# Optimization experiments

Hardware: AMD Instinct MI355X
Metric: run time of the kernel (lower is better)

The kernel has to match this reference:

```python
import jax, jax.numpy as jnp
import numpy as np

N = 2048      # num graph nodes (activities + places)
D = 256       # embedding_size
C = 3 * D     # cat_embedding_size
V = 2         # num variants
L = 16        # activities per variant
E = 16 * N    # edges for the encoder GNN
DEG_P = 0.0156  # adjacency density (~32 out-degree)


def setup_inputs() -> dict:
    key = jax.random.key(0)
    ks = jax.random.split(key, 6)
    embeddings = jax.random.normal(ks[0], (N, D), dtype=jnp.float32)
    W_self = jax.random.normal(ks[1], (D, D), dtype=jnp.float32) * 0.05
    W_nbr = jax.random.normal(ks[2], (D, D), dtype=jnp.float32) * 0.05
    b = jnp.zeros((D,), dtype=jnp.float32)
    variants = jax.random.randint(ks[3], (V, L), 0, N, dtype=jnp.int32)
    original = (jax.random.uniform(ks[4], (N, N)) < DEG_P).astype(jnp.int32)
    edge_index = jax.random.randint(ks[5], (2, E), 0, N, dtype=jnp.int32)
    return {"embeddings": embeddings, "W_self": W_self, "W_nbr": W_nbr, "b": b,
            "variants": variants, "original": original, "edge_index": edge_index}


def _forward(embeddings, W_self, W_nbr, b, variants, original, edge_index):
    n, d = embeddings.shape
    c = 3 * d
    dt = embeddings.dtype
    adj = original.astype(dt)              # [N,N]; adj[i,j]=1 iff edge i->j (forward star = row)
    src_e, dst_e = edge_index[0], edge_index[1]

    def encoder(x):
        # SecondEncoder approximated as one GCN-style message-passing layer
        msg = jax.ops.segment_sum(x[src_e], dst_e, num_segments=n)
        return jax.nn.relu(x @ W_self + msg @ W_nbr + b)

    def run_variant(acts):  # acts: [L] int32
        onehot = jax.nn.one_hot(acts, n, dtype=dt)                # [L,N]
        incl = jnp.flip(jnp.cumsum(jnp.flip(onehot, 0), 0), 0)    # sum_{j>=i} onehot[j]
        present_later = ((incl - onehot) > 0).astype(dt)          # set of nodes in acts[i+1:]

        def step(carry, inp):
            emb, pi, summary = carry
            a, plater = inp
            followers = adj[a]                                    # forward star of activity a
            has = jnp.any(followers > 0)
            adj_m = adj * plater[None, :]                         # edges into later-in-variant activities
            dest_cnt = adj_m.sum(axis=1)                          # |destination set| per candidate place
            dst_all = adj_m @ emb                                 # summed destination embeddings, [N,D]
            mask = jnp.where(has, ((followers > 0) & (dest_cnt > 0)).astype(dt), 0.0)
            # cat = (place_f, src_f, dst_f) per considered place
            cat = jnp.concatenate(
                [emb, jnp.broadcast_to(emb[a][None, :], emb.shape), dst_all], axis=1) * mask[:, None]
            pi = pi + cat                                         # places_info[place] += cat
            # prev_embedding_summary += places_info[place] for each considered place
            summary = summary + (mask[:, None] * pi).sum(axis=0)
            # places_info[considered] += prev_embedding_summary
            pi = pi + mask[:, None] * summary[None, :]
            emb = jnp.where(has, encoder(emb), emb)               # encoder skipped when no followers
            return (emb, pi, summary), None

        init = (embeddings, jnp.zeros((n, c), dt), jnp.zeros((c,), dt))
        (_, pi, _), _ = jax.lax.scan(step, init, (acts, present_later))
        return pi

    # variant shuffle in the original is irrelevant: embeddings reset each variant
    # and final_places_info is a sum over variants.
    return jax.vmap(run_variant)(variants).sum(axis=0)


def reference(embeddings, W_self, W_nbr, b, variants, original, edge_index):
    return _forward(embeddings, W_self, W_nbr, b, variants, original, edge_index)
```

## Files before the change

kernel.cpp:

```cpp
#include <hip/hip_runtime.h>

#define N 2048
#define D 256
#define C 768
#define V 2
#define L 16
#define NSTATE 15
#define NAPP 14
#define TCAP 256
#define FCAP 64

typedef __attribute__((ext_vector_type(8))) short bf16x8;
typedef __attribute__((ext_vector_type(4))) float f32x4;

__device__ __forceinline__ ushort bf16_rn(float x) {
  unsigned u = __float_as_uint(x);
  u += 0x7FFFu + ((u >> 16) & 1u);
  return (ushort)(u >> 16);
}
__device__ __forceinline__ float bf16_f(ushort h) {
  return __uint_as_float(((unsigned)h) << 16);
}

__device__ __forceinline__ size_t a_addr(int row, int k) {
  return ((size_t)(row >> 5) * 4 + (k >> 6)) * 2048 + (row & 31) * 64 + (k & 63);
}
__device__ __forceinline__ size_t wt_addr(int n, int k) {
  return ((size_t)(n >> 5) * 4 + (k >> 6)) * 2048 + (n & 31) * 64 + (k & 63);
}

__global__ __launch_bounds__(256) void k_init(
    const float* __restrict__ emb, const float* __restrict__ Ws,
    const float* __restrict__ Wn, float* __restrict__ states0,
    ushort* __restrict__ WtHi, ushort* __restrict__ WtLo,
    ushort* __restrict__ A0hi, ushort* __restrict__ A0lo,
    float* __restrict__ out, int* __restrict__ fillpos) {
  size_t i = (size_t)blockIdx.x * 256 + threadIdx.x;
  size_t stride = (size_t)gridDim.x * 256;
  for (size_t x = i; x < (size_t)N * D; x += stride) {
    float v = emb[x];
    states0[x] = v;
    ushort h = bf16_rn(v);
    ushort l = bf16_rn(v - bf16_f(h));
    size_t a = a_addr((int)(x >> 8), (int)(x & 255));
    A0hi[a] = h;
    A0lo[a] = l;
  }
  for (size_t x = i; x < (size_t)512 * 256; x += stride) {
    int n = (int)(x >> 8), k = (int)(x & 255);
    float v = (n < 256) ? Ws[(size_t)k * 256 + n] : Wn[(size_t)k * 256 + (n - 256)];
    ushort h = bf16_rn(v);
    size_t a = wt_addr(n, k);
    WtHi[a] = h;
    WtLo[a] = bf16_rn(v - bf16_f(h));
  }
  for (size_t x = i; x < (size_t)N * C; x += stride) out[x] = 0.f;
  for (size_t x = i; x < N; x += stride) fillpos[x] = 0;
}

__global__ void k_deg(const int* __restrict__ ei, int* __restrict__ fillpos, int E) {
  int e = blockIdx.x * 256 + threadIdx.x;
  if (e < E) atomicAdd(&fillpos[ei[E + e]], 1);
}

__global__ __launch_bounds__(256) void k_scan(int* __restrict__ fillpos,
                                              int* __restrict__ row_ptr) {
  __shared__ int part[256];
  __shared__ int base[257];
  int t = threadIdx.x;
  int v[8];
  int s = 0;
  for (int j = 0; j < 8; j++) { v[j] = fillpos[t * 8 + j]; s += v[j]; }
  part[t] = s;
  __syncthreads();
  if (t == 0) {
    int acc = 0;
    for (int q = 0; q < 256; q++) { base[q] = acc; acc += part[q]; }
    base[256] = acc;
  }
  __syncthreads();
  int acc = base[t];
  for (int j = 0; j < 8; j++) {
    row_ptr[t * 8 + j] = acc;
    fillpos[t * 8 + j] = acc;
    acc += v[j];
  }
  if (t == 255) row_ptr[N] = base[256];
}

__global__ void k_fill(const int* __restrict__ ei, int* __restrict__ fillpos,
                       int* __restrict__ csr_src, int E) {
  int e = blockIdx.x * 256 + threadIdx.x;
  if (e < E) {
    int dst = ei[E + e];
    int pos = atomicAdd(&fillpos[dst], 1);
    csr_src[pos] = ei[e];
  }
}

__global__ __launch_bounds__(256) void k_metaA(
    const int* __restrict__ adj, const int* __restrict__ variants,
    int* __restrict__ stepP, int* __restrict__ stepDm,
    int* __restrict__ stepCnt, int* __restrict__ hasG, int* __restrict__ tlG) {
  __shared__ int tl_sh[16];
  __shared__ int foll[FCAP], fbits[FCAP];
  __shared__ int sh_tc, sh_fcnt, sh_ecnt;
  int vi = blockIdx.x;
  int v = vi / L, i = vi % L;
  int t = threadIdx.x;
  int a = variants[vi];
  if (t == 0) {
    int cnt = 0;
    for (int j = i + 1; j < L; j++) {
      int x = variants[v * L + j];
      bool dup = false;
      for (int q = 0; q < cnt; q++) if (tl_sh[q] == x) dup = true;
      if (!dup) tl_sh[cnt++] = x;
    }
    sh_tc = cnt;
    sh_fcnt = 0;
    sh_ecnt = 0;
    for (int q = 0; q < cnt; q++) tlG[vi * 16 + q] = tl_sh[q];
  }
  __syncthreads();
  for (int p = t; p < N; p += 256) {
    if (adj[(size_t)a * N + p] != 0) {
      int f = atomicAdd(&sh_fcnt, 1);
      if (f < FCAP) foll[f] = p;
    }
  }
  __syncthreads();
  int fc = sh_fcnt < FCAP ? sh_fcnt : FCAP;
  int tc = sh_tc;
  for (int x = t; x < fc; x += 256) fbits[x] = 0;
  __syncthreads();
  for (int x = t; x < fc * tc; x += 256) {
    int fi = x / tc, q = x - fi * tc;
    if (adj[(size_t)foll[fi] * N + tl_sh[q]] != 0) atomicOr(&fbits[fi], 1 << q);
  }
  __syncthreads();
  for (int fi = t; fi < fc; fi += 256) {
    int bits = fbits[fi];
    if (bits) {
      int e = atomicAdd(&sh_ecnt, 1);
      stepP[vi * FCAP + e] = foll[fi];
      stepDm[vi * FCAP + e] = bits;
    }
  }
  __syncthreads();
  if (t == 0) {
    stepCnt[vi] = sh_ecnt;
    hasG[vi] = (sh_fcnt > 0);
  }
}

__global__ __launch_bounds__(256) void k_metaB(
    const int* __restrict__ stepP, const int* __restrict__ stepDm,
    const int* __restrict__ stepCnt, const int* __restrict__ hasG,
    int* __restrict__ entP, int* __restrict__ entPrev, int* __restrict__ entDm,
    int* __restrict__ offsG, int* __restrict__ kidxG, int* __restrict__ cmatG,
    int* __restrict__ lastPG, int* __restrict__ lastIG, int* __restrict__ lastMG,
    int* __restrict__ cntG) {
  __shared__ int pmask[N];
  __shared__ int sP[16][FCAP];
  __shared__ int sDm[16][FCAP];
  __shared__ int cnt[16], offs[17];
  __shared__ int cmat_sh[256];
  __shared__ int sh_u;
  int v = blockIdx.x, t = threadIdx.x;
  for (int p = t; p < N; p += 256) pmask[p] = 0;
  for (int x = t; x < 256; x += 256) cmat_sh[x] = 0;
  if (t < 16) cnt[t] = stepCnt[v * L + t];
  if (t == 0) sh_u = 0;
  __syncthreads();
  if (t == 0) {
    int acc = 0;
    for (int i = 0; i < 16; i++) {
      offs[i] = acc < TCAP ? acc : TCAP;
      acc += cnt[i];
    }
    offs[16] = acc < TCAP ? acc : TCAP;
    cntG[v * 2 + 0] = offs[16];
    int k = 0;
    for (int i = 0; i < L; i++) {
      kidxG[v * 16 + i] = k;
      if (hasG[v * L + i]) k++;
    }
  }
  for (int x = t; x < 16 * FCAP; x += 256) {
    int i = x >> 6, f = x & 63;
    if (f < stepCnt[v * L + i]) {
      int p = stepP[(v * L + i) * FCAP + f];
      sP[i][f] = p;
      sDm[i][f] = stepDm[(v * L + i) * FCAP + f];
      atomicOr(&pmask[p], 1 << i);
    }
  }
  __syncthreads();
  for (int x = t; x < 16 * FCAP; x += 256) {
    int i = x >> 6, f = x & 63;
    if (f < cnt[i]) {
      int e = offs[i] + f;
      if (e < TCAP) {
        int p = sP[i][f];
        entP[v * TCAP + e] = p;
        entDm[v * TCAP + e] = sDm[i][f];
        int m = pmask[p] & ((1 << i) - 1);
        int prev = -1;
        if (m) {
          int j = 31 - __clz(m);
          int cj = cnt[j];
          for (int f2 = 0; f2 < cj; f2++)
            if (sP[j][f2] == p) { prev = offs[j] + f2; break; }
        }
        entPrev[v * TCAP + e] = prev;
      }
    }
  }
  __syncthreads();
  for (int p = t; p < N; p += 256) {
    int m = pmask[p];
    if (m) {
      int u = atomicAdd(&sh_u, 1);
      int j = 31 - __clz(m);
      int li = -1;
      int cj = cnt[j];
      for (int f2 = 0; f2 < cj; f2++)
        if (sP[j][f2] == p) { li = offs[j] + f2; break; }
      lastPG[v * TCAP + u] = p;
      lastIG[v * TCAP + u] = li;
      lastMG[v * TCAP + u] = m;
      int mm = m;
      while (mm) {
        int bi = __ffs(mm) - 1; mm &= mm - 1;
        int m2 = m & ((1 << bi) - 1);
        while (m2) {
          int bj = __ffs(m2) - 1; m2 &= m2 - 1;
          atomicAdd(&cmat_sh[bi * 16 + bj], 1);
        }
      }
    }
  }
  __syncthreads();
  if (t == 0) cntG[v * 2 + 1] = sh_u;
  for (int x = t; x < 256; x += 256) cmatG[v * 256 + x] = cmat_sh[x];
  for (int x = t; x < 17; x += 256) offsG[v * 17 + x] = offs[x];
}

__global__ __launch_bounds__(256) void k_gemm(
    const ushort* __restrict__ Ah, const ushort* __restrict__ Al,
    const ushort* __restrict__ Wh_g, const ushort* __restrict__ Wl_g,
    float* __restrict__ Z) {
  __shared__ __align__(16) ushort Ash[32][72], Asl[32][72];
  __shared__ __align__(16) ushort Wsh[32][72], Wsl[32][72];
  const int tid = threadIdx.x, wave = tid >> 6, lane = tid & 63;
  const int quad = lane >> 4, l16 = lane & 15;
  const int wr = wave >> 1, wc = wave & 1;
  const int mb = blockIdx.x, nb = blockIdx.y;
  const int sr = tid >> 3, sc = (tid & 7) * 8;

  f32x4 acc = {0.f, 0.f, 0.f, 0.f};
  size_t abase = (size_t)mb * 4 * 2048 + (size_t)tid * 8;
  size_t wbase = (size_t)nb * 4 * 2048 + (size_t)tid * 8;
  uint4 ra  = *(const uint4*)&Ah[abase];
  uint4 rl  = *(const uint4*)&Al[abase];
  uint4 rwh = *(const uint4*)&Wh_g[wbase];
  uint4 rwl = *(const uint4*)&Wl_g[wbase];
#pragma unroll
  for (int c = 0; c < 4; c++) {
    *(uint4*)&Ash[sr][sc] = ra;
    *(uint4*)&Asl[sr][sc] = rl;
    *(uint4*)&Wsh[sr][sc] = rwh;
    *(uint4*)&Wsl[sr][sc] = rwl;
    __syncthreads();
    if (c < 3) {
      size_t o = (size_t)(c + 1) * 2048;
      ra  = *(const uint4*)&Ah[abase + o];
      rl  = *(const uint4*)&Al[abase + o];
      rwh = *(const uint4*)&Wh_g[wbase + o];
      rwl = *(const uint4*)&Wl_g[wbase + o];
    }
#pragma unroll
    for (int kf = 0; kf < 2; kf++) {
      int ko = kf * 32 + quad * 8;
      bf16x8 a_h = *(const bf16x8*)&Ash[wr * 16 + l16][ko];
      bf16x8 a_l = *(const bf16x8*)&Asl[wr * 16 + l16][ko];
      bf16x8 w_h = *(const bf16x8*)&Wsh[wc * 16 + l16][ko];
      bf16x8 w_l = *(const bf16x8*)&Wsl[wc * 16 + l16][ko];
      acc = __builtin_amdgcn_mfma_f32_16x16x32_bf16(a_h, w_h, acc, 0, 0, 0);
      acc = __builtin_amdgcn_mfma_f32_16x16x32_bf16(a_h, w_l, acc, 0, 0, 0);
      acc = __builtin_amdgcn_mfma_f32_16x16x32_bf16(a_l, w_h, acc, 0, 0, 0);
    }
    __syncthreads();
  }
  int col = nb * 32 + wc * 16 + l16;
  int row0 = mb * 32 + wr * 16 + quad * 4;
#pragma unroll
  for (int r = 0; r < 4; r++)
    Z[(size_t)(row0 + r) * 512 + col] = acc[r];
}

__global__ __launch_bounds__(256) void k_comb(
    const float* __restrict__ Z, const float* __restrict__ bias,
    const int* __restrict__ row_ptr, const int* __restrict__ csr_src,
    float* __restrict__ stnext, ushort* __restrict__ NAh,
    ushort* __restrict__ NAl) {
  __shared__ float4 part[2][64];
  int wid = threadIdx.x >> 6, lane = threadIdx.x & 63;
  int rp = wid >> 1, half = wid & 1;
  int row = blockIdx.x * 2 + rp;
  int e0 = row_ptr[row], e1 = row_ptr[row + 1];
  int mid = (e0 + e1 + 1) >> 1;
  int lo = half ? mid : e0, hi = half ? e1 : mid;
  float4 acc = {0.f, 0.f, 0.f, 0.f};
  for (int e = lo; e < hi; e++) {
    const float4* z2 = (const float4*)(Z + (size_t)csr_src[e] * 512 + 256);
    float4 x = z2[lane];
    acc.x += x.x; acc.y += x.y; acc.z += x.z; acc.w += x.w;
  }
  if (half) part[rp][lane] = acc;
  __syncthreads();
  if (!half) {
    float4 o = part[rp][lane];
    float4 zs = ((const float4*)(Z + (size_t)row * 512))[lane];
    float4 bv = ((const float4*)bias)[lane];
    float v0 = fmaxf(acc.x + o.x + zs.x + bv.x, 0.f);
    float v1 = fmaxf(acc.y + o.y + zs.y + bv.y, 0.f);
    float v2 = fmaxf(acc.z + o.z + zs.z + bv.z, 0.f);
    float v3 = fmaxf(acc.w + o.w + zs.w + bv.w, 0.f);
    *(float4*)(stnext + (size_t)row * D + lane * 4) = make_float4(v0, v1, v2, v3);
    ushort h0 = bf16_rn(v0), h1 = bf16_rn(v1), h2 = bf16_rn(v2), h3 = bf16_rn(v3);
    size_t ca = a_addr(row, lane * 4);
    *(ushort4*)&NAh[ca] = make_ushort4(h0, h1, h2, h3);
    *(ushort4*)&NAl[ca] = make_ushort4(
        bf16_rn(v0 - bf16_f(h0)), bf16_rn(v1 - bf16_f(h1)),
        bf16_rn(v2 - bf16_f(h2)), bf16_rn(v3 - bf16_f(h3)));
  }
}

#define PI_LDS_BYTES (TCAP * 64 * 4 + 16 * 64 * 4 + 3 * TCAP * 4 + 17 * 4 + 16 * 4 + 256 * 4)
__global__ __launch_bounds__(64) void k_pi(
    const float* __restrict__ states, float* __restrict__ out,
    const int* __restrict__ variants,
    const int* __restrict__ entP, const int* __restrict__ entPrev,
    const int* __restrict__ entDm, const int* __restrict__ offsG,
    const int* __restrict__ kidxG, const int* __restrict__ tlG,
    const int* __restrict__ cmatG, const int* __restrict__ lastPG,
    const int* __restrict__ lastIG, const int* __restrict__ lastMG,
    const int* __restrict__ cntG) {
  extern __shared__ __align__(16) float smf[];
  float* catb = smf;
  float* S_lds = catb + TCAP * 64;
  int* eP  = (int*)(S_lds + 16 * 64);
  int* ePr = eP + TCAP;
  int* eDm = ePr + TCAP;
  int* offs = eDm + TCAP;
  int* kidx = offs + 17;
  int* tl = kidx + 16;
  int v = blockIdx.x / 12, cgi = blockIdx.x % 12;
  int grp = cgi >> 2;
  int lane = threadIdx.x;
  int cl = (cgi & 3) * 64 + lane;
  int col = cgi * 64 + lane;

  int T = cntG[v * 2 + 0], U = cntG[v * 2 + 1];
  for (int x = lane; x < T; x += 64) {
    eP[x] = entP[v * TCAP + x];
    ePr[x] = entPrev[v * TCAP + x];
    eDm[x] = entDm[v * TCAP + x];
  }
  for (int x = lane; x < 17; x += 64) offs[x] = offsG[v * 17 + x];
  if (lane < 16) kidx[lane] = kidxG[v * 16 + lane];
  for (int x = lane; x < 256; x += 64) tl[x] = tlG[v * 256 + x];
  __syncthreads();

  for (int i = 0; i < L; i++) {
    int kk = kidx[i]; if (kk > NSTATE - 1) kk = NSTATE - 1;
    const float* embS = states + (size_t)kk * N * D;
    int o0 = offs[i], o1 = offs[i + 1];
    if (grp == 0) {
      for (int e = o0; e < o1; e++)
        catb[e * 64 + lane] = embS[(size_t)eP[e] * D + cl];
    } else if (grp == 1) {
      float embA = embS[(size_t)variants[v * L + i] * D + cl];
      for (int e = o0; e < o1; e++) catb[e * 64 + lane] = embA;
    } else {
      for (int e = o0; e < o1; e++) {
        float s = 0.f;
        int b = eDm[e];
        while (b) {
          int q = __ffs(b) - 1; b &= b - 1;
          s += embS[(size_t)tl[i * 16 + q] * D + cl];
        }
        catb[e * 64 + lane] = s;
      }
    }
  }
  for (int e = 0; e < T; e++) {
    int pr = ePr[e];
    if (pr >= 0) catb[e * 64 + lane] += catb[pr * 64 + lane];
  }
  float S[16];
  float Sp = 0.f;
#pragma unroll
  for (int i = 0; i < 16; i++) {
    float a = 0.f;
    for (int e = offs[i]; e < offs[i + 1]; e++) a += catb[e * 64 + lane];
    float s = Sp + a;
#pragma unroll
    for (int j = 0; j < 16; j++)
      if (j < i) s += (float)cmatG[v * 256 + i * 16 + j] * S[j];
    S[i] = s;
    S_lds[i * 64 + lane] = s;
    Sp = s;
  }
  for (int u = 0; u < U; u++) {
    int p = lastPG[v * TCAP + u];
    int li = lastIG[v * TCAP + u];
    int m = lastMG[v * TCAP + u];
    float acc = catb[li * 64 + lane];
    while (m) {
      int q = __ffs(m) - 1; m &= m - 1;
      acc += S_lds[q * 64 + lane];
    }
    atomicAdd(&out[(size_t)p * C + col], acc);
  }
}

extern "C" void kernel_launch(void* const* d_in, const int* in_sizes, int n_in,
                              void* d_out, int out_size, void* d_ws, size_t ws_size,
                              hipStream_t stream) {
  const float* emb      = (const float*)d_in[0];
  const float* Ws       = (const float*)d_in[1];
  const float* Wn       = (const float*)d_in[2];
  const float* bias     = (const float*)d_in[3];
  const int*   variants = (const int*)d_in[4];
  const int*   adj      = (const int*)d_in[5];
  const int*   ei       = (const int*)d_in[6];
  const int    E        = in_sizes[6] / 2;
  float* out            = (float*)d_out;

  char* base = (char*)d_ws;
  float* states = (float*)base;            base += (size_t)NSTATE * N * D * 4;
  float* Z      = (float*)base;            base += (size_t)N * 512 * 4;
  ushort* WtHi  = (ushort*)base;           base += (size_t)512 * 256 * 2;
  ushort* WtLo  = (ushort*)base;           base += (size_t)512 * 256 * 2;
  ushort* A0h   = (ushort*)base;           base += (size_t)N * D * 2;
  ushort* A0l   = (ushort*)base;           base += (size_t)N * D * 2;
  ushort* A1h   = (ushort*)base;           base += (size_t)N * D * 2;
  ushort* A1l   = (ushort*)base;           base += (size_t)N * D * 2;
  int* row_ptr  = (int*)base;              base += (N + 1) * 4;
  int* fillpos  = (int*)base;              base += N * 4;
  int* csr_src  = (int*)base;              base += (size_t)E * 4;
  int* stepP    = (int*)base;              base += V * L * FCAP * 4;
  int* stepDm   = (int*)base;              base += V * L * FCAP * 4;
  int* stepCnt  = (int*)base;              base += V * L * 4;
  int* hasG     = (int*)base;              base += V * L * 4;
  int* entP     = (int*)base;              base += V * TCAP * 4;
  int* entPrev  = (int*)base;              base += V * TCAP * 4;
  int* entDm    = (int*)base;              base += V * TCAP * 4;
  int* offsG    = (int*)base;              base += V * 17 * 4;
  int* kidxG    = (int*)base;              base += V * 16 * 4;
  int* tlG      = (int*)base;              base += V * 256 * 4;
  int* cmatG    = (int*)base;              base += V * 256 * 4;
  int* lastPG   = (int*)base;              base += V * TCAP * 4;
  int* lastIG   = (int*)base;              base += V * TCAP * 4;
  int* lastMG   = (int*)base;              base += V * TCAP * 4;
  int* cntG     = (int*)base;              base += V * 2 * 4;

  hipFuncSetAttribute((const void*)k_pi,
                      hipFuncAttributeMaxDynamicSharedMemorySize, PI_LDS_BYTES);

  k_init<<<512, 256, 0, stream>>>(emb, Ws, Wn, states, WtHi, WtLo, A0h, A0l,
                                  out, fillpos);
  k_deg<<<(E + 255) / 256, 256, 0, stream>>>(ei, fillpos, E);
  k_scan<<<1, 256, 0, stream>>>(fillpos, row_ptr);
  k_fill<<<(E + 255) / 256, 256, 0, stream>>>(ei, fillpos, csr_src, E);
  k_metaA<<<V * L, 256, 0, stream>>>(adj, variants, stepP, stepDm, stepCnt,
                                     hasG, tlG);
  k_metaB<<<V, 256, 0, stream>>>(stepP, stepDm, stepCnt, hasG, entP, entPrev,
                                 entDm, offsG, kidxG, cmatG, lastPG, lastIG,
                                 lastMG, cntG);

  ushort* AH[2] = {A0h, A1h};
  ushort* AL[2] = {A0l, A1l};
  for (int s = 0; s < NAPP; s++) {
    int cur = s & 1, nxt = cur ^ 1;
    k_gemm<<<dim3(64, 16), 256, 0, stream>>>(AH[cur], AL[cur], WtHi, WtLo, Z);
    k_comb<<<N / 2, 256, 0, stream>>>(Z, bias, row_ptr, csr_src,
                                      states + (size_t)(s + 1) * N * D,
                                      AH[nxt], AL[nxt]);
  }
  k_pi<<<V * 12, 64, PI_LDS_BYTES, stream>>>(states, out, variants, entP,
                                             entPrev, entDm, offsG, kidxG, tlG,
                                             cmatG, lastPG, lastIG, lastMG, cntG);
}
```

Measured before the change: 386.9 us.

## Merge setup kernels, double-buffer GEMM LDS, simplify per-row gather combine

Merges the degree-count kernel with the per-step metadata kernel, and the CSR fill kernel with the per-variant metadata kernel, by splitting blocks by index. This cuts the number of launches. The GEMM now double-buffers its LDS tiles, so each k-chunk needs one barrier instead of two. The combine kernel now runs one wave per row with two independent accumulators instead of splitting each row across two waves with an LDS reduction. The extra LDS in the GEMM and the loss of intra-row parallelism on high-degree rows may offset part of the benefit.

```diff
diff --git a/kernel.cpp b/kernel.cpp
--- a/kernel.cpp
+++ b/kernel.cpp
@@ -58,9 +58,66 @@
   for (size_t x = i; x < N; x += stride) fillpos[x] = 0;
 }
 
-__global__ void k_deg(const int* __restrict__ ei, int* __restrict__ fillpos, int E) {
-  int e = blockIdx.x * 256 + threadIdx.x;
-  if (e < E) atomicAdd(&fillpos[ei[E + e]], 1);
+__global__ __launch_bounds__(256) void k_degA(
+    const int* __restrict__ ei, int E, int* __restrict__ fillpos,
+    const int* __restrict__ adj, const int* __restrict__ variants,
+    int* __restrict__ stepP, int* __restrict__ stepDm,
+    int* __restrict__ stepCnt, int* __restrict__ hasG, int* __restrict__ tlG) {
+  __shared__ int tl_sh[16];
+  __shared__ int foll[FCAP], fbits[FCAP];
+  __shared__ int sh_tc, sh_fcnt, sh_ecnt;
+  int t = threadIdx.x;
+  if (blockIdx.x < 128) {
+    for (int e = blockIdx.x * 256 + t; e < E; e += 128 * 256)
+      atomicAdd(&fillpos[ei[E + e]], 1);
+    return;
+  }
+  int vi = blockIdx.x - 128;
+  int v = vi / L, i = vi % L;
+  int a = variants[vi];
+  if (t == 0) {
+    int cnt = 0;
+    for (int j = i + 1; j < L; j++) {
+      int x = variants[v * L + j];
+      bool dup = false;
+      for (int q = 0; q < cnt; q++) if (tl_sh[q] == x) dup = true;
+      if (!dup) tl_sh[cnt++] = x;
+    }
+    sh_tc = cnt;
+    sh_fcnt = 0;
+    sh_ecnt = 0;
+    for (int q = 0; q < cnt; q++) tlG[vi * 16 + q] = tl_sh[q];
+  }
+  __syncthreads();
+  for (int p = t; p < N; p += 256) {
+    if (adj[(size_t)a * N + p] != 0) {
+      int f = atomicAdd(&sh_fcnt, 1);
+      if (f < FCAP) foll[f] = p;
+    }
+  }
+  __syncthreads();
+  int fc = sh_fcnt < FCAP ? sh_fcnt : FCAP;
+  int tc = sh_tc;
+  for (int x = t; x < fc; x += 256) fbits[x] = 0;
+  __syncthreads();
+  for (int x = t; x < fc * tc; x += 256) {
+    int fi = x / tc, q = x - fi * tc;
+    if (adj[(size_t)foll[fi] * N + tl_sh[q]] != 0) atomicOr(&fbits[fi], 1 << q);
+  }
+  __syncthreads();
+  for (int fi = t; fi < fc; fi += 256) {
+    int bits = fbits[fi];
+    if (bits) {
+      int e = atomicAdd(&sh_ecnt, 1);
+      stepP[vi * FCAP + e] = foll[fi];
+      stepDm[vi * FCAP + e] = bits;
+    }
+  }
+  __syncthreads();
+  if (t == 0) {
+    stepCnt[vi] = sh_ecnt;
+    hasG[vi] = (sh_fcnt > 0);
+  }
 }
 
 __global__ __launch_bounds__(256) void k_scan(int* __restrict__ fillpos,
@@ -88,73 +145,9 @@
   if (t == 255) row_ptr[N] = base[256];
 }
 
-__global__ void k_fill(const int* __restrict__ ei, int* __restrict__ fillpos,
-                       int* __restrict__ csr_src, int E) {
-  int e = blockIdx.x * 256 + threadIdx.x;
-  if (e < E) {
-    int dst = ei[E + e];
-    int pos = atomicAdd(&fillpos[dst], 1);
-    csr_src[pos] = ei[e];
-  }
-}
-
-__global__ __launch_bounds__(256) void k_metaA(
-    const int* __restrict__ adj, const int* __restrict__ variants,
-    int* __restrict__ stepP, int* __restrict__ stepDm,
-    int* __restrict__ stepCnt, int* __restrict__ hasG, int* __restrict__ tlG) {
-  __shared__ int tl_sh[16];
-  __shared__ int foll[FCAP], fbits[FCAP];
-  __shared__ int sh_tc, sh_fcnt, sh_ecnt;
-  int vi = blockIdx.x;
-  int v = vi / L, i = vi % L;
-  int t = threadIdx.x;
-  int a = variants[vi];
-  if (t == 0) {
-    int cnt = 0;
-    for (int j = i + 1; j < L; j++) {
-      int x = variants[v * L + j];
-      bool dup = false;
-      for (int q = 0; q < cnt; q++) if (tl_sh[q] == x) dup = true;
-      if (!dup) tl_sh[cnt++] = x;
-    }
-    sh_tc = cnt;
-    sh_fcnt = 0;
-    sh_ecnt = 0;
-    for (int q = 0; q < cnt; q++) tlG[vi * 16 + q] = tl_sh[q];
-  }
-  __syncthreads();
-  for (int p = t; p < N; p += 256) {
-    if (adj[(size_t)a * N + p] != 0) {
-      int f = atomicAdd(&sh_fcnt, 1);
-      if (f < FCAP) foll[f] = p;
-    }
-  }
-  __syncthreads();
-  int fc = sh_fcnt < FCAP ? sh_fcnt : FCAP;
-  int tc = sh_tc;
-  for (int x = t; x < fc; x += 256) fbits[x] = 0;
-  __syncthreads();
-  for (int x = t; x < fc * tc; x += 256) {
-    int fi = x / tc, q = x - fi * tc;
-    if (adj[(size_t)foll[fi] * N + tl_sh[q]] != 0) atomicOr(&fbits[fi], 1 << q);
-  }
-  __syncthreads();
-  for (int fi = t; fi < fc; fi += 256) {
-    int bits = fbits[fi];
-    if (bits) {
-      int e = atomicAdd(&sh_ecnt, 1);
-      stepP[vi * FCAP + e] = foll[fi];
-      stepDm[vi * FCAP + e] = bits;
-    }
-  }
-  __syncthreads();
-  if (t == 0) {
-    stepCnt[vi] = sh_ecnt;
-    hasG[vi] = (sh_fcnt > 0);
-  }
-}
-
-__global__ __launch_bounds__(256) void k_metaB(
+__global__ __launch_bounds__(256) void k_fillB(
+    const int* __restrict__ ei, int E, int* __restrict__ fillpos,
+    int* __restrict__ csr_src,
     const int* __restrict__ stepP, const int* __restrict__ stepDm,
     const int* __restrict__ stepCnt, const int* __restrict__ hasG,
     int* __restrict__ entP, int* __restrict__ entPrev, int* __restrict__ entDm,
@@ -167,7 +160,16 @@
   __shared__ int cnt[16], offs[17];
   __shared__ int cmat_sh[256];
   __shared__ int sh_u;
-  int v = blockIdx.x, t = threadIdx.x;
+  int t = threadIdx.x;
+  if (blockIdx.x < 128) {
+    for (int e = blockIdx.x * 256 + t; e < E; e += 128 * 256) {
+      int dst = ei[E + e];
+      int pos = atomicAdd(&fillpos[dst], 1);
+      csr_src[pos] = ei[e];
+    }
+    return;
+  }
+  int v = blockIdx.x - 128;
   for (int p = t; p < N; p += 256) pmask[p] = 0;
   for (int x = t; x < 256; x += 256) cmat_sh[x] = 0;
   if (t < 16) cnt[t] = stepCnt[v * L + t];
@@ -251,8 +253,8 @@
     const ushort* __restrict__ Ah, const ushort* __restrict__ Al,
     const ushort* __restrict__ Wh_g, const ushort* __restrict__ Wl_g,
     float* __restrict__ Z) {
-  __shared__ __align__(16) ushort Ash[32][72], Asl[32][72];
-  __shared__ __align__(16) ushort Wsh[32][72], Wsl[32][72];
+  __shared__ __align__(16) ushort Ash[2][32][72], Asl[2][32][72];
+  __shared__ __align__(16) ushort Wsh[2][32][72], Wsl[2][32][72];
   const int tid = threadIdx.x, wave = tid >> 6, lane = tid & 63;
   const int quad = lane >> 4, l16 = lane & 15;
   const int wr = wave >> 1, wc = wave & 1;
@@ -262,17 +264,21 @@
   f32x4 acc = {0.f, 0.f, 0.f, 0.f};
   size_t abase = (size_t)mb * 4 * 2048 + (size_t)tid * 8;
   size_t wbase = (size_t)nb * 4 * 2048 + (size_t)tid * 8;
-  uint4 ra  = *(const uint4*)&Ah[abase];
-  uint4 rl  = *(const uint4*)&Al[abase];
-  uint4 rwh = *(const uint4*)&Wh_g[wbase];
-  uint4 rwl = *(const uint4*)&Wl_g[wbase];
+  {
+    uint4 ra  = *(const uint4*)&Ah[abase];
+    uint4 rl  = *(const uint4*)&Al[abase];
+    uint4 rwh = *(const uint4*)&Wh_g[wbase];
+    uint4 rwl = *(const uint4*)&Wl_g[wbase];
+    *(uint4*)&Ash[0][sr][sc] = ra;
+    *(uint4*)&Asl[0][sr][sc] = rl;
+    *(uint4*)&Wsh[0][sr][sc] = rwh;
+    *(uint4*)&Wsl[0][sr][sc] = rwl;
+  }
+  __syncthreads();
 #pragma unroll
   for (int c = 0; c < 4; c++) {
-    *(uint4*)&Ash[sr][sc] = ra;
-    *(uint4*)&Asl[sr][sc] = rl;
-    *(uint4*)&Wsh[sr][sc] = rwh;
-    *(uint4*)&Wsl[sr][sc] = rwl;
-    __syncthreads();
+    const int rb = c & 1;
+    uint4 ra, rl, rwh, rwl;
     if (c < 3) {
       size_t o = (size_t)(c + 1) * 2048;
       ra  = *(const uint4*)&Ah[abase + o];
@@ -283,15 +289,22 @@
 #pragma unroll
     for (int kf = 0; kf < 2; kf++) {
       int ko = kf * 32 + quad * 8;
-      bf16x8 a_h = *(const bf16x8*)&Ash[wr * 16 + l16][ko];
-      bf16x8 a_l = *(const bf16x8*)&Asl[wr * 16 + l16][ko];
-      bf16x8 w_h = *(const bf16x8*)&Wsh[wc * 16 + l16][ko];
-      bf16x8 w_l = *(const bf16x8*)&Wsl[wc * 16 + l16][ko];
+      bf16x8 a_h = *(const bf16x8*)&Ash[rb][wr * 16 + l16][ko];
+      bf16x8 a_l = *(const bf16x8*)&Asl[rb][wr * 16 + l16][ko];
+      bf16x8 w_h = *(const bf16x8*)&Wsh[rb][wc * 16 + l16][ko];
+      bf16x8 w_l = *(const bf16x8*)&Wsl[rb][wc * 16 + l16][ko];
       acc = __builtin_amdgcn_mfma_f32_16x16x32_bf16(a_h, w_h, acc, 0, 0, 0);
       acc = __builtin_amdgcn_mfma_f32_16x16x32_bf16(a_h, w_l, acc, 0, 0, 0);
       acc = __builtin_amdgcn_mfma_f32_16x16x32_bf16(a_l, w_h, acc, 0, 0, 0);
     }
-    __syncthreads();
+    if (c < 3) {
+      const int wb = rb ^ 1;
+      *(uint4*)&Ash[wb][sr][sc] = ra;
+      *(uint4*)&Asl[wb][sr][sc] = rl;
+      *(uint4*)&Wsh[wb][sr][sc] = rwh;
+      *(uint4*)&Wsl[wb][sr][sc] = rwl;
+      __syncthreads();
+    }
   }
   int col = nb * 32 + wc * 16 + l16;
   int row0 = mb * 32 + wr * 16 + quad * 4;
@@ -305,37 +318,36 @@
     const int* __restrict__ row_ptr, const int* __restrict__ csr_src,
     float* __restrict__ stnext, ushort* __restrict__ NAh,
     ushort* __restrict__ NAl) {
-  __shared__ float4 part[2][64];
-  int wid = threadIdx.x >> 6, lane = threadIdx.x & 63;
-  int rp = wid >> 1, half = wid & 1;
-  int row = blockIdx.x * 2 + rp;
+  int row = blockIdx.x * 4 + (threadIdx.x >> 6);
+  int lane = threadIdx.x & 63;
+  const float4* Zp = (const float4*)Z;
+  float4 acc = Zp[(size_t)row * 128 + lane];
+  float4 acc2 = {0.f, 0.f, 0.f, 0.f};
   int e0 = row_ptr[row], e1 = row_ptr[row + 1];
-  int mid = (e0 + e1 + 1) >> 1;
-  int lo = half ? mid : e0, hi = half ? e1 : mid;
-  float4 acc = {0.f, 0.f, 0.f, 0.f};
-  for (int e = lo; e < hi; e++) {
-    const float4* z2 = (const float4*)(Z + (size_t)csr_src[e] * 512 + 256);
-    float4 x = z2[lane];
-    acc.x += x.x; acc.y += x.y; acc.z += x.z; acc.w += x.w;
-  }
-  if (half) part[rp][lane] = acc;
-  __syncthreads();
-  if (!half) {
-    float4 o = part[rp][lane];
-    float4 zs = ((const float4*)(Z + (size_t)row * 512))[lane];
-    float4 bv = ((const float4*)bias)[lane];
-    float v0 = fmaxf(acc.x + o.x + zs.x + bv.x, 0.f);
-    float v1 = fmaxf(acc.y + o.y + zs.y + bv.y, 0.f);
-    float v2 = fmaxf(acc.z + o.z + zs.z + bv.z, 0.f);
-    float v3 = fmaxf(acc.w + o.w + zs.w + bv.w, 0.f);
-    *(float4*)(stnext + (size_t)row * D + lane * 4) = make_float4(v0, v1, v2, v3);
-    ushort h0 = bf16_rn(v0), h1 = bf16_rn(v1), h2 = bf16_rn(v2), h3 = bf16_rn(v3);
-    size_t ca = a_addr(row, lane * 4);
-    *(ushort4*)&NAh[ca] = make_ushort4(h0, h1, h2, h3);
-    *(ushort4*)&NAl[ca] = make_ushort4(
-        bf16_rn(v0 - bf16_f(h0)), bf16_rn(v1 - bf16_f(h1)),
-        bf16_rn(v2 - bf16_f(h2)), bf16_rn(v3 - bf16_f(h3)));
-  }
+  int e = e0;
+  for (; e + 1 < e1; e += 2) {
+    int s0 = csr_src[e], s1 = csr_src[e + 1];
+    float4 x0 = Zp[(size_t)s0 * 128 + 64 + lane];
+    float4 x1 = Zp[(size_t)s1 * 128 + 64 + lane];
+    acc.x += x0.x; acc.y += x0.y; acc.z += x0.z; acc.w += x0.w;
+    acc2.x += x1.x; acc2.y += x1.y; acc2.z += x1.z; acc2.w += x1.w;
+  }
+  if (e < e1) {
+    float4 x0 = Zp[(size_t)csr_src[e] * 128 + 64 + lane];
+    acc.x += x0.x; acc.y += x0.y; acc.z += x0.z; acc.w += x0.w;
+  }
+  float4 bv = ((const float4*)bias)[lane];
+  float v0 = fmaxf(acc.x + acc2.x + bv.x, 0.f);
+  float v1 = fmaxf(acc.y + acc2.y + bv.y, 0.f);
+  float v2 = fmaxf(acc.z + acc2.z + bv.z, 0.f);
+  float v3 = fmaxf(acc.w + acc2.w + bv.w, 0.f);
+  *(float4*)(stnext + (size_t)row * D + lane * 4) = make_float4(v0, v1, v2, v3);
+  ushort h0 = bf16_rn(v0), h1 = bf16_rn(v1), h2 = bf16_rn(v2), h3 = bf16_rn(v3);
+  size_t ca = a_addr(row, lane * 4);
+  *(ushort4*)&NAh[ca] = make_ushort4(h0, h1, h2, h3);
+  *(ushort4*)&NAl[ca] = make_ushort4(
+      bf16_rn(v0 - bf16_f(h0)), bf16_rn(v1 - bf16_f(h1)),
+      bf16_rn(v2 - bf16_f(h2)), bf16_rn(v3 - bf16_f(h3)));
 }
 
 #define PI_LDS_BYTES (TCAP * 64 * 4 + 16 * 64 * 4 + 3 * TCAP * 4 + 17 * 4 + 16 * 4 + 256 * 4)
@@ -473,21 +485,20 @@
 
   k_init<<<512, 256, 0, stream>>>(emb, Ws, Wn, states, WtHi, WtLo, A0h, A0l,
                                   out, fillpos);
-  k_deg<<<(E + 255) / 256, 256, 0, stream>>>(ei, fillpos, E);
+  k_degA<<<128 + V * L, 256, 0, stream>>>(ei, E, fillpos, adj, variants,
+                                          stepP, stepDm, stepCnt, hasG, tlG);
   k_scan<<<1, 256, 0, stream>>>(fillpos, row_ptr);
-  k_fill<<<(E + 255) / 256, 256, 0, stream>>>(ei, fillpos, csr_src, E);
-  k_metaA<<<V * L, 256, 0, stream>>>(adj, variants, stepP, stepDm, stepCnt,
-                                     hasG, tlG);
-  k_metaB<<<V, 256, 0, stream>>>(stepP, stepDm, stepCnt, hasG, entP, entPrev,
-                                 entDm, offsG, kidxG, cmatG, lastPG, lastIG,
-                                 lastMG, cntG);
+  k_fillB<<<128 + V, 256, 0, stream>>>(ei, E, fillpos, csr_src, stepP, stepDm,
+                                       stepCnt, hasG, entP, entPrev, entDm,
+                                       offsG, kidxG, cmatG, lastPG, lastIG,
+                                       lastMG, cntG);
 
   ushort* AH[2] = {A0h, A1h};
   ushort* AL[2] = {A0l, A1l};
   for (int s = 0; s < NAPP; s++) {
     int cur = s & 1, nxt = cur ^ 1;
     k_gemm<<<dim3(64, 16), 256, 0, stream>>>(AH[cur], AL[cur], WtHi, WtLo, Z);
-    k_comb<<<N / 2, 256, 0, stream>>>(Z, bias, row_ptr, csr_src,
+    k_comb<<<N / 4, 256, 0, stream>>>(Z, bias, row_ptr, csr_src,
                                       states + (size_t)(s + 1) * N * D,
                                       AH[nxt], AL[nxt]);
   }
```

Result: no change. 380.0 us (-1.8%).
